# Performance work log

Hardware: AMD Instinct MI355X
Metric: run time of the kernel (lower is better)

The kernel has to match this reference:

```python
import jax, jax.numpy as jnp
import numpy as np

N = 65536        # total points across batch
NS = 16          # nsample (kNN neighbors)
D = 64           # d_model
FF = 64          # dim_feedforward width
CIN = 16         # input feature channels
EPS = 1e-5       # BatchNorm eps


def _bn_relu(x, g, b):
    # BatchNorm1d in training mode: per-channel stats over (N, L); x: (N, C, L)
    m = x.mean(axis=(0, 2), keepdims=True)
    v = x.var(axis=(0, 2), keepdims=True)
    return jax.nn.relu((x - m) * jax.lax.rsqrt(v + EPS) * g[None, :, None] + b[None, :, None])


def _dknn_layer(xyz, feats, knn_idx, knn_empty,
                wq, bq, wk, bk, w1, g1, b1, w2, g2, b2, wo, go, bo):
    # nhead = 1 -> single head uses the full d_model split
    Q = feats @ wq + bq                        # (N, D)
    K = feats @ wk + bk                        # (N, D)
    Kx = jnp.concatenate([K, xyz], axis=1)     # use_xyz=True -> (N, D+3)
    Qx = jnp.concatenate([Q, xyz], axis=1)     # (N, D+3)
    Kg = jnp.transpose(Kx[knn_idx], (0, 2, 1))  # irregular gather -> (N, D+3, NS)
    Qe = Qx[:, :, None]                        # (N, D+3, 1)
    x = jnp.concatenate([Kg - Qe, jnp.broadcast_to(Qe, Kg.shape)], axis=1)  # (N, 2*(D+3), NS)
    x = jnp.where(knn_empty[:, None, None], 0.0, x)   # empty-ball masking
    x = _bn_relu(jnp.einsum('ncs,cf->nfs', x, w1), g1, b1)  # Conv1d k=1 == channel matmul
    x = _bn_relu(jnp.einsum('ncs,cf->nfs', x, w2), g2, b2)
    x = jnp.max(x, axis=2, keepdims=True)      # max-pool over neighbors -> (N, FF, 1)
    x = _bn_relu(jnp.einsum('ncs,cf->nfs', x, wo), go, bo)  # out_conv
    return x[:, :, 0]                          # (N, D)


def setup_inputs() -> dict:
    key = jax.random.key(0)
    ks = jax.random.split(key, 16)
    inp = {
        'src_xyz': jax.random.normal(ks[0], (N, 3), jnp.float32) * 20.0,
        'src_feats': jax.random.normal(ks[1], (N, CIN), jnp.float32),
        'knn_idx': jax.random.randint(ks[2], (N, NS), 0, N, jnp.int32),
        'knn_empty': jax.random.randint(ks[3], (N,), 0, 20, jnp.int32) == 0,
    }
    k = 4
    cin = CIN
    for i in range(2):
        s = 1.0 / np.sqrt(cin)
        inp[f'l{i}_wq'] = jax.random.normal(ks[k], (cin, D), jnp.float32) * s; k += 1
        inp[f'l{i}_bq'] = jnp.zeros((D,), jnp.float32)
        inp[f'l{i}_wk'] = jax.random.normal(ks[k], (cin, D), jnp.float32) * s; k += 1
        inp[f'l{i}_bk'] = jnp.zeros((D,), jnp.float32)
        c = 2 * (D + 3)
        inp[f'l{i}_w1'] = jax.random.normal(ks[k], (c, FF), jnp.float32) * np.sqrt(2.0 / c); k += 1
        inp[f'l{i}_g1'] = jnp.ones((FF,), jnp.float32)
        inp[f'l{i}_b1'] = jnp.zeros((FF,), jnp.float32)
        inp[f'l{i}_w2'] = jax.random.normal(ks[k], (FF, FF), jnp.float32) * np.sqrt(2.0 / FF); k += 1
        inp[f'l{i}_g2'] = jnp.ones((FF,), jnp.float32)
        inp[f'l{i}_b2'] = jnp.zeros((FF,), jnp.float32)
        inp[f'l{i}_wo'] = jax.random.normal(ks[k], (FF, D), jnp.float32) * np.sqrt(2.0 / FF); k += 1
        inp[f'l{i}_go'] = jnp.ones((D,), jnp.float32)
        inp[f'l{i}_bo'] = jnp.zeros((D,), jnp.float32)
        cin = D
    return inp


def reference(src_xyz, src_feats, knn_idx, knn_empty,
              l0_wq, l0_bq, l0_wk, l0_bk, l0_w1, l0_g1, l0_b1, l0_w2, l0_g2, l0_b2, l0_wo, l0_go, l0_bo,
              l1_wq, l1_bq, l1_wk, l1_bk, l1_w1, l1_g1, l1_b1, l1_w2, l1_g2, l1_b2, l1_wo, l1_go, l1_bo):
    f = _dknn_layer(src_xyz, src_feats, knn_idx, knn_empty,
                    l0_wq, l0_bq, l0_wk, l0_bk, l0_w1, l0_g1, l0_b1, l0_w2, l0_g2, l0_b2, l0_wo, l0_go, l0_bo)
    f = _dknn_layer(src_xyz, f, knn_idx, knn_empty,
                    l1_wq, l1_bq, l1_wk, l1_bk, l1_w1, l1_g1, l1_b1, l1_w2, l1_g2, l1_b2, l1_wo, l1_go, l1_bo)
    return f
```

## Files before the change

### kernel.cpp

```cpp
#include <hip/hip_runtime.h>
#include <cstdint>

#define NPTS 65536
#define NS 16
#define EPSV 1e-5f

typedef __attribute__((ext_vector_type(8))) short bf16x8;
typedef __attribute__((ext_vector_type(4))) float f32x4;
typedef __attribute__((ext_vector_type(4))) unsigned int u32x4;
union FragU { u32x4 u; bf16x8 h; };

#define SUM1 0
#define SSQ1 64
#define SUM2 128
#define SSQ2 192
#define SUM3 256
#define SSQ3 320
#define WKAOF 0
#define WQBAOF 4096
#define BKAOF 8192
#define BQBAOF 8256
#define WFOLD_FLOATS 8320

__device__ __forceinline__ void split2(float e0, float e1, unsigned int& hi, unsigned int& lo) {
    unsigned int u0 = __float_as_uint(e0), u1 = __float_as_uint(e1);
    unsigned int h0 = u0 & 0xFFFF0000u, h1 = u1 & 0xFFFF0000u;
    hi = (h0 >> 16) | h1;
    float l0f = e0 - __uint_as_float(h0);
    float l1f = e1 - __uint_as_float(h1);
    lo = (__float_as_uint(l0f) >> 16) | (__float_as_uint(l1f) & 0xFFFF0000u);
}

__global__ void k_mask(const uint32_t* emp32, uint8_t* mask) {
    int bad = 0;
    for (int w = threadIdx.x; w < 1024; w += 256) bad |= (emp32[w] > 1u) ? 1 : 0;
    __shared__ int sbad[4];
    unsigned long long b = __ballot(bad != 0);
    if ((threadIdx.x & 63) == 0) sbad[threadIdx.x >> 6] = (b != 0ull) ? 1 : 0;
    __syncthreads();
    int flag = sbad[0] | sbad[1] | sbad[2] | sbad[3];
    int i = blockIdx.x * 256 + threadIdx.x;
    uint8_t mv;
    if (flag) mv = (((const uint8_t*)emp32)[i] != 0);
    else      mv = (emp32[i] != 0u);
    mask[i] = mv;
}

__global__ void k0(const float* wq, const float* bq, const float* wk, const float* bk,
                   const float* w1, float* wfold, int cin) {
    int f = threadIdx.x;
    int c = blockIdx.x;
    float a = 0.f, q = 0.f;
    for (int d = 0; d < 64; d++) {
        float A  = w1[d*64 + f];
        float Bm = w1[(67+d)*64 + f] - A;
        a = fmaf(wk[c*64 + d], A,  a);
        q = fmaf(wq[c*64 + d], Bm, q);
    }
    wfold[WKAOF  + c*64 + f] = a;
    wfold[WQBAOF + c*64 + f] = q;
    if (c == 0) {
        float ba = 0.f, bqv = 0.f;
        for (int d = 0; d < 64; d++) {
            float A  = w1[d*64 + f];
            float Bm = w1[(67+d)*64 + f] - A;
            ba  = fmaf(bk[d], A,  ba);
            bqv = fmaf(bq[d], Bm, bqv);
        }
        wfold[BKAOF  + f] = ba;
        wfold[BQBAOF + f] = bqv;
    }
}

template<int CIN, bool PREBN>
__global__ void __launch_bounds__(256) k1m(const float* __restrict__ feats, const float* __restrict__ xyz,
                    const float* __restrict__ w1, const float* __restrict__ wfold,
                    const float* __restrict__ statsPrev, const float* __restrict__ goP,
                    const float* __restrict__ boP,
                    float* __restrict__ KA, float* __restrict__ QBA) {
    const int l = threadIdx.x & 63;
    const int wv = threadIdx.x >> 6;
    const int sidx = l & 15;
    const int g = l >> 4;
    const int col = sidx;
    constexpr int NT = (CIN == 64) ? 2 : 1;

    unsigned int bh[NT][2][4], bl[NT][2][4];
    #pragma unroll
    for (int t = 0; t < NT; t++)
    #pragma unroll
    for (int fl = 0; fl < 2; fl++) {
        int f128 = (wv*2 + fl)*16 + col;
        const float* W = (f128 < 64) ? (wfold + WKAOF) : (wfold + WQBAOF);
        int f = (f128 < 64) ? f128 : f128 - 64;
        #pragma unroll
        for (int r = 0; r < 4; r++) {
            int c0 = t*32 + g*8 + 2*r;
            float e0 = 0.f, e1 = 0.f;
            if (CIN == 64 || g < 2) {
                e0 = W[c0*64 + f];
                e1 = W[(c0+1)*64 + f];
            }
            split2(e0, e1, bh[t][fl][r], bl[t][fl][r]);
        }
    }
    unsigned int xbh[2][4], xbl[2][4];
    float biasf[2];
    #pragma unroll
    for (int fl = 0; fl < 2; fl++) {
        int f128 = (wv*2 + fl)*16 + col;
        float A0, A1, A2;
        if (f128 < 64) {
            A0 = w1[64*64 + f128]; A1 = w1[65*64 + f128]; A2 = w1[66*64 + f128];
            biasf[fl] = wfold[BKAOF + f128];
        } else {
            int f = f128 - 64;
            A0 = w1[131*64 + f] - w1[64*64 + f];
            A1 = w1[132*64 + f] - w1[65*64 + f];
            A2 = w1[133*64 + f] - w1[66*64 + f];
            biasf[fl] = wfold[BQBAOF + f];
        }
        split2(A0, A1, xbh[fl][0], xbl[fl][0]);
        split2(A2, 0.f, xbh[fl][1], xbl[fl][1]);
        xbh[fl][2] = 0; xbh[fl][3] = 0; xbl[fl][2] = 0; xbl[fl][3] = 0;
    }
    float scP[NT*8], shP[NT*8];
    if (PREBN) {
        const float invN = 1.0f / (float)NPTS;
        #pragma unroll
        for (int t = 0; t < NT; t++)
        #pragma unroll
        for (int i = 0; i < 8; i++) {
            int c = t*32 + g*8 + i;
            float m = statsPrev[SUM3 + c] * invN;
            float v = fmaxf(statsPrev[SSQ3 + c] * invN - m*m, 0.0f);
            float s = goP[c] * rsqrtf(v + EPSV);
            scP[t*8+i] = s;
            shP[t*8+i] = fmaf(-m, s, boP[c]);
        }
    }

    for (int tile = blockIdx.x; tile < NPTS/16; tile += gridDim.x) {
        int p = tile*16 + sidx;
        unsigned int ahu[NT][4], alu[NT][4];
        #pragma unroll
        for (int t = 0; t < NT; t++) {
            float xv[8];
            if (CIN == 64) {
                f32x4 a0 = *(const f32x4*)(feats + (size_t)p*64 + t*32 + g*8);
                f32x4 a1 = *(const f32x4*)(feats + (size_t)p*64 + t*32 + g*8 + 4);
                #pragma unroll
                for (int i = 0; i < 4; i++) { xv[i] = a0[i]; xv[4+i] = a1[i]; }
                if (PREBN) {
                    #pragma unroll
                    for (int i = 0; i < 8; i++)
                        xv[i] = fmaxf(fmaf(scP[t*8+i], xv[i], shP[t*8+i]), 0.0f);
                }
            } else {
                if (g < 2) {
                    f32x4 a0 = *(const f32x4*)(feats + (size_t)p*16 + g*8);
                    f32x4 a1 = *(const f32x4*)(feats + (size_t)p*16 + g*8 + 4);
                    #pragma unroll
                    for (int i = 0; i < 4; i++) { xv[i] = a0[i]; xv[4+i] = a1[i]; }
                } else {
                    #pragma unroll
                    for (int i = 0; i < 8; i++) xv[i] = 0.f;
                }
            }
            #pragma unroll
            for (int r = 0; r < 4; r++) split2(xv[2*r], xv[2*r+1], ahu[t][r], alu[t][r]);
        }
        unsigned int xah[4] = {0,0,0,0}, xal[4] = {0,0,0,0};
        if (g == 0) {
            float x0 = xyz[p*3], x1 = xyz[p*3+1], x2 = xyz[p*3+2];
            split2(x0, x1, xah[0], xal[0]);
            split2(x2, 0.f, xah[1], xal[1]);
        }
        f32x4 acc[2];
        #pragma unroll
        for (int fl = 0; fl < 2; fl++)
            acc[fl] = (f32x4){biasf[fl], biasf[fl], biasf[fl], biasf[fl]};
        #pragma unroll
        for (int t = 0; t < NT; t++) {
            FragU ah, al;
            ah.u = (u32x4){ahu[t][0], ahu[t][1], ahu[t][2], ahu[t][3]};
            al.u = (u32x4){alu[t][0], alu[t][1], alu[t][2], alu[t][3]};
            #pragma unroll
            for (int fl = 0; fl < 2; fl++) {
                FragU Bh, Bl;
                Bh.u = (u32x4){bh[t][fl][0], bh[t][fl][1], bh[t][fl][2], bh[t][fl][3]};
                Bl.u = (u32x4){bl[t][fl][0], bl[t][fl][1], bl[t][fl][2], bl[t][fl][3]};
                acc[fl] = __builtin_amdgcn_mfma_f32_16x16x32_bf16(ah.h, Bh.h, acc[fl], 0, 0, 0);
                acc[fl] = __builtin_amdgcn_mfma_f32_16x16x32_bf16(ah.h, Bl.h, acc[fl], 0, 0, 0);
                acc[fl] = __builtin_amdgcn_mfma_f32_16x16x32_bf16(al.h, Bh.h, acc[fl], 0, 0, 0);
            }
        }
        {
            FragU ah, al;
            ah.u = (u32x4){xah[0], xah[1], xah[2], xah[3]};
            al.u = (u32x4){xal[0], xal[1], xal[2], xal[3]};
            #pragma unroll
            for (int fl = 0; fl < 2; fl++) {
                FragU Bh, Bl;
                Bh.u = (u32x4){xbh[fl][0], xbh[fl][1], xbh[fl][2], xbh[fl][3]};
                Bl.u = (u32x4){xbl[fl][0], xbl[fl][1], xbl[fl][2], xbl[fl][3]};
                acc[fl] = __builtin_amdgcn_mfma_f32_16x16x32_bf16(ah.h, Bh.h, acc[fl], 0, 0, 0);
                acc[fl] = __builtin_amdgcn_mfma_f32_16x16x32_bf16(ah.h, Bl.h, acc[fl], 0, 0, 0);
                acc[fl] = __builtin_amdgcn_mfma_f32_16x16x32_bf16(al.h, Bh.h, acc[fl], 0, 0, 0);
            }
        }
        #pragma unroll
        for (int fl = 0; fl < 2; fl++) {
            int f128 = (wv*2 + fl)*16 + col;
            #pragma unroll
            for (int r = 0; r < 4; r++) {
                int po = tile*16 + g*4 + r;
                float v = acc[fl][r];
                if (f128 < 64) KA[(size_t)po*64 + f128] = v;
                else           QBA[(size_t)po*64 + (f128-64)] = v;
            }
        }
    }
}

__global__ void __launch_bounds__(256) k2(const float* __restrict__ KA, const float* __restrict__ QBA,
                   const int* __restrict__ knn, const uint8_t* __restrict__ mask, float* stats) {
    const int l = threadIdx.x & 63;
    const int wv = threadIdx.x >> 6;
    const int s = l & 15;
    const int g = l >> 4;
    float s0[16], s1[16];
    #pragma unroll
    for (int i = 0; i < 16; i++) { s0[i] = 0.f; s1[i] = 0.f; }
    for (int n = blockIdx.x * 4 + wv; n < NPTS; n += gridDim.x * 4) {
        if (mask[n]) continue;
        int j = knn[n*16 + s];
        const float* kap = KA + (size_t)j*64 + g*16;
        const float* qbp = QBA + (size_t)n*64 + g*16;
        #pragma unroll
        for (int q = 0; q < 4; q++) {
            f32x4 ka = *(const f32x4*)(kap + q*4);
            f32x4 qb = *(const f32x4*)(qbp + q*4);
            #pragma unroll
            for (int e = 0; e < 4; e++) {
                float y = ka[e] + qb[e];
                s0[q*4+e] += y;
                s1[q*4+e] = fmaf(y, y, s1[q*4+e]);
            }
        }
    }
    #pragma unroll
    for (int i = 0; i < 16; i++) {
        #pragma unroll
        for (int d = 1; d < 16; d <<= 1) {
            s0[i] += __shfl_xor(s0[i], d, 64);
            s1[i] += __shfl_xor(s1[i], d, 64);
        }
    }
    __shared__ float r0[4][64], r1[4][64];
    if (s == 0) {
        #pragma unroll
        for (int i = 0; i < 16; i++) { r0[wv][g*16+i] = s0[i]; r1[wv][g*16+i] = s1[i]; }
    }
    __syncthreads();
    int tid = threadIdx.x;
    if (tid < 64) {
        atomicAdd(&stats[SUM1 + tid], r0[0][tid]+r0[1][tid]+r0[2][tid]+r0[3][tid]);
        atomicAdd(&stats[SSQ1 + tid], r1[0][tid]+r1[1][tid]+r1[2][tid]+r1[3][tid]);
    }
}

__global__ void __launch_bounds__(256) k4(const float* KA, const float* QBA, const int* knn,
                   const uint8_t* mask, const float* w2, const float* g1, const float* b1,
                   float* stats, float* y2max, float* y2min) {
    const int l    = threadIdx.x & 63;
    const int wv   = threadIdx.x >> 6;
    const int sidx = l & 15;
    const int g    = l >> 4;
    const int col  = sidx;

    float sc1v[16], sh1v[16];
    const float inv = 1.0f / ((float)NPTS * (float)NS);
    #pragma unroll
    for (int t = 0; t < 2; t++)
    #pragma unroll
    for (int i = 0; i < 8; i++) {
        int c = t*32 + g*8 + i;
        float m = stats[SUM1 + c] * inv;
        float v = fmaxf(stats[SSQ1 + c] * inv - m*m, 0.0f);
        float s = g1[c] * rsqrtf(v + EPSV);
        sc1v[t*8+i] = s;
        sh1v[t*8+i] = fmaf(-m, s, b1[c]);
    }

    unsigned int whu[2][4][4], wlu[2][4][4];
    #pragma unroll
    for (int t = 0; t < 2; t++)
    #pragma unroll
    for (int ft = 0; ft < 4; ft++)
    #pragma unroll
    for (int r = 0; r < 4; r++) {
        int k0i = t*32 + g*8 + 2*r;
        float e0 = w2[k0i*64 + ft*16 + col];
        float e1 = w2[(k0i+1)*64 + ft*16 + col];
        split2(e0, e1, whu[t][ft][r], wlu[t][ft][r]);
    }

    float s0t[4] = {0.f,0.f,0.f,0.f};
    float s1t[4] = {0.f,0.f,0.f,0.f};

    for (int n = blockIdx.x * 4 + wv; n < NPTS; n += gridDim.x * 4) {
        bool masked = mask[n] != 0;
        int j = knn[n*16 + sidx];

        f32x4 kaA = *(const f32x4*)(KA + (size_t)j*64 + g*8);
        f32x4 kaB = *(const f32x4*)(KA + (size_t)j*64 + g*8 + 4);
        f32x4 kaC = *(const f32x4*)(KA + (size_t)j*64 + 32 + g*8);
        f32x4 kaD = *(const f32x4*)(KA + (size_t)j*64 + 32 + g*8 + 4);
        f32x4 qA  = *(const f32x4*)(QBA + (size_t)n*64 + g*8);
        f32x4 qB  = *(const f32x4*)(QBA + (size_t)n*64 + g*8 + 4);
        f32x4 qC  = *(const f32x4*)(QBA + (size_t)n*64 + 32 + g*8);
        f32x4 qD  = *(const f32x4*)(QBA + (size_t)n*64 + 32 + g*8 + 4);

        float x[16];
        #pragma unroll
        for (int i = 0; i < 4; i++) {
            float y0 = masked ? 0.f : (kaA[i] + qA[i]);
            float y1 = masked ? 0.f : (kaB[i] + qB[i]);
            float y2 = masked ? 0.f : (kaC[i] + qC[i]);
            float y3 = masked ? 0.f : (kaD[i] + qD[i]);
            x[i]    = fmaxf(fmaf(sc1v[i],    y0, sh1v[i]),    0.0f);
            x[4+i]  = fmaxf(fmaf(sc1v[4+i],  y1, sh1v[4+i]),  0.0f);
            x[8+i]  = fmaxf(fmaf(sc1v[8+i],  y2, sh1v[8+i]),  0.0f);
            x[12+i] = fmaxf(fmaf(sc1v[12+i], y3, sh1v[12+i]), 0.0f);
        }

        unsigned int ahu[2][4], alu[2][4];
        #pragma unroll
        for (int t = 0; t < 2; t++)
        #pragma unroll
        for (int r = 0; r < 4; r++)
            split2(x[t*8 + 2*r], x[t*8 + 2*r + 1], ahu[t][r], alu[t][r]);

        f32x4 acc[4];
        #pragma unroll
        for (int ft = 0; ft < 4; ft++) acc[ft] = (f32x4){0.f,0.f,0.f,0.f};

        #pragma unroll
        for (int t = 0; t < 2; t++) {
            FragU ah, al;
            ah.u = (u32x4){ahu[t][0], ahu[t][1], ahu[t][2], ahu[t][3]};
            al.u = (u32x4){alu[t][0], alu[t][1], alu[t][2], alu[t][3]};
            #pragma unroll
            for (int ft = 0; ft < 4; ft++) {
                FragU bhf, blf;
                bhf.u = (u32x4){whu[t][ft][0], whu[t][ft][1], whu[t][ft][2], whu[t][ft][3]};
                blf.u = (u32x4){wlu[t][ft][0], wlu[t][ft][1], wlu[t][ft][2], wlu[t][ft][3]};
                acc[ft] = __builtin_amdgcn_mfma_f32_16x16x32_bf16(ah.h, bhf.h, acc[ft], 0, 0, 0);
                acc[ft] = __builtin_amdgcn_mfma_f32_16x16x32_bf16(ah.h, blf.h, acc[ft], 0, 0, 0);
                acc[ft] = __builtin_amdgcn_mfma_f32_16x16x32_bf16(al.h, bhf.h, acc[ft], 0, 0, 0);
            }
        }

        float tmax[4], tmin[4];
        #pragma unroll
        for (int ft = 0; ft < 4; ft++) {
            f32x4 d = acc[ft];
            float lmax = fmaxf(fmaxf(d[0], d[1]), fmaxf(d[2], d[3]));
            float lmin = fminf(fminf(d[0], d[1]), fminf(d[2], d[3]));
            s0t[ft] += (d[0] + d[1]) + (d[2] + d[3]);
            s1t[ft] += fmaf(d[0],d[0], fmaf(d[1],d[1], fmaf(d[2],d[2], d[3]*d[3])));
            lmax = fmaxf(lmax, __shfl_xor(lmax, 16, 64));
            lmax = fmaxf(lmax, __shfl_xor(lmax, 32, 64));
            lmin = fminf(lmin, __shfl_xor(lmin, 16, 64));
            lmin = fminf(lmin, __shfl_xor(lmin, 32, 64));
            tmax[ft] = lmax; tmin[ft] = lmin;
        }
        float mx = (g==0) ? tmax[0] : (g==1) ? tmax[1] : (g==2) ? tmax[2] : tmax[3];
        float mn = (g==0) ? tmin[0] : (g==1) ? tmin[1] : (g==2) ? tmin[2] : tmin[3];
        y2max[(size_t)n*64 + l] = mx;
        y2min[(size_t)n*64 + l] = mn;
    }

    #pragma unroll
    for (int ft = 0; ft < 4; ft++) {
        s0t[ft] += __shfl_xor(s0t[ft], 16, 64);
        s0t[ft] += __shfl_xor(s0t[ft], 32, 64);
        s1t[ft] += __shfl_xor(s1t[ft], 16, 64);
        s1t[ft] += __shfl_xor(s1t[ft], 32, 64);
    }
    float myS0 = (g==0) ? s0t[0] : (g==1) ? s0t[1] : (g==2) ? s0t[2] : s0t[3];
    float myS1 = (g==0) ? s1t[0] : (g==1) ? s1t[1] : (g==2) ? s1t[2] : s1t[3];
    __shared__ float red[8][64];
    red[wv][l] = myS0;
    red[4+wv][l] = myS1;
    __syncthreads();
    if (wv == 0) {
        atomicAdd(&stats[SUM2 + l], red[0][l]+red[1][l]+red[2][l]+red[3][l]);
        atomicAdd(&stats[SSQ2 + l], red[4][l]+red[5][l]+red[6][l]+red[7][l]);
    }
}

__global__ void __launch_bounds__(256) k5m(const float* __restrict__ y2max, const float* __restrict__ y2min,
                    const float* __restrict__ wo, const float* __restrict__ g2, const float* __restrict__ b2,
                    float* stats, float* __restrict__ y3) {
    const int l = threadIdx.x & 63;
    const int wv = threadIdx.x >> 6;
    const int sidx = l & 15;
    const int g = l >> 4;
    const int ft = wv;

    unsigned int bh[2][4], bl[2][4];
    #pragma unroll
    for (int t = 0; t < 2; t++)
    #pragma unroll
    for (int r = 0; r < 4; r++) {
        int c0 = t*32 + g*8 + 2*r;
        split2(wo[c0*64 + ft*16 + sidx], wo[(c0+1)*64 + ft*16 + sidx], bh[t][r], bl[t][r]);
    }
    float sc2v[16], sh2v[16];
    const float inv = 1.0f / ((float)NPTS * (float)NS);
    #pragma unroll
    for (int t = 0; t < 2; t++)
    #pragma unroll
    for (int i = 0; i < 8; i++) {
        int c = t*32 + g*8 + i;
        float m = stats[SUM2 + c] * inv;
        float v = fmaxf(stats[SSQ2 + c] * inv - m*m, 0.0f);
        float s = g2[c] * rsqrtf(v + EPSV);
        sc2v[t*8+i] = s;
        sh2v[t*8+i] = fmaf(-m, s, b2[c]);
    }
    float s0a = 0.f, s1a = 0.f;
    for (int tile = blockIdx.x; tile < NPTS/16; tile += gridDim.x) {
        int p = tile*16 + sidx;
        unsigned int ahu[2][4], alu[2][4];
        #pragma unroll
        for (int t = 0; t < 2; t++) {
            f32x4 mx0 = *(const f32x4*)(y2max + (size_t)p*64 + t*32 + g*8);
            f32x4 mx1 = *(const f32x4*)(y2max + (size_t)p*64 + t*32 + g*8 + 4);
            f32x4 mn0 = *(const f32x4*)(y2min + (size_t)p*64 + t*32 + g*8);
            f32x4 mn1 = *(const f32x4*)(y2min + (size_t)p*64 + t*32 + g*8 + 4);
            float mval[8];
            #pragma unroll
            for (int i = 0; i < 4; i++) {
                float sc = sc2v[t*8+i];
                float pre = (sc >= 0.f) ? mx0[i] : mn0[i];
                mval[i] = fmaxf(fmaf(sc, pre, sh2v[t*8+i]), 0.0f);
                float sc2 = sc2v[t*8+4+i];
                float pre2 = (sc2 >= 0.f) ? mx1[i] : mn1[i];
                mval[4+i] = fmaxf(fmaf(sc2, pre2, sh2v[t*8+4+i]), 0.0f);
            }
            #pragma unroll
            for (int r = 0; r < 4; r++) split2(mval[2*r], mval[2*r+1], ahu[t][r], alu[t][r]);
        }
        f32x4 acc = (f32x4){0.f,0.f,0.f,0.f};
        #pragma unroll
        for (int t = 0; t < 2; t++) {
            FragU ah, al, Bh, Bl;
            ah.u = (u32x4){ahu[t][0], ahu[t][1], ahu[t][2], ahu[t][3]};
            al.u = (u32x4){alu[t][0], alu[t][1], alu[t][2], alu[t][3]};
            Bh.u = (u32x4){bh[t][0], bh[t][1], bh[t][2], bh[t][3]};
            Bl.u = (u32x4){bl[t][0], bl[t][1], bl[t][2], bl[t][3]};
            acc = __builtin_amdgcn_mfma_f32_16x16x32_bf16(ah.h, Bh.h, acc, 0, 0, 0);
            acc = __builtin_amdgcn_mfma_f32_16x16x32_bf16(ah.h, Bl.h, acc, 0, 0, 0);
            acc = __builtin_amdgcn_mfma_f32_16x16x32_bf16(al.h, Bh.h, acc, 0, 0, 0);
        }
        #pragma unroll
        for (int r = 0; r < 4; r++) {
            int po = tile*16 + g*4 + r;
            float v = acc[r];
            y3[(size_t)po*64 + ft*16 + sidx] = v;
            s0a += v;
            s1a = fmaf(v, v, s1a);
        }
    }
    s0a += __shfl_xor(s0a, 16, 64); s0a += __shfl_xor(s0a, 32, 64);
    s1a += __shfl_xor(s1a, 16, 64); s1a += __shfl_xor(s1a, 32, 64);
    __shared__ float r0[64], r1[64];
    if (l < 16) { r0[wv*16 + sidx] = s0a; r1[wv*16 + sidx] = s1a; }
    __syncthreads();
    int tid = threadIdx.x;
    if (tid < 64) {
        atomicAdd(&stats[SUM3 + tid], r0[tid]);
        atomicAdd(&stats[SSQ3 + tid], r1[tid]);
    }
}

__global__ void k6(float* y3, const float* stats, const float* go, const float* bo) {
    int i = blockIdx.x * 256 + threadIdx.x;
    int f = i & 63;
    const float inv = 1.0f / (float)NPTS;
    float m = stats[SUM3 + f] * inv;
    float v = fmaxf(stats[SSQ3 + f] * inv - m*m, 0.0f);
    float s = go[f] * rsqrtf(v + EPSV);
    float sh = fmaf(-m, s, bo[f]);
    y3[i] = fmaxf(fmaf(s, y3[i], sh), 0.0f);
}

extern "C" void kernel_launch(void* const* d_in, const int* in_sizes, int n_in,
                              void* d_out, int out_size, void* d_ws, size_t ws_size,
                              hipStream_t stream) {
    const float* xyz    = (const float*)d_in[0];
    const float* feats0 = (const float*)d_in[1];
    const int*   knn    = (const int*)d_in[2];
    const void*  empty  = d_in[3];
    float* ws = (float*)d_ws;
    const size_t N64 = (size_t)NPTS * 64;
    float* KA    = ws;
    float* QBA   = ws + N64;
    float* Y2MAX = ws + 2*N64;
    float* Y2MIN = ws + 3*N64;
    float* stats = ws + 4*N64;
    float* wfold = stats + 1024;
    uint8_t* mask = (uint8_t*)(wfold + WFOLD_FLOATS);
    float* out = (float*)d_out;

    hipMemsetAsync(stats, 0, 1024 * sizeof(float), stream);
    k_mask<<<NPTS/256, 256, 0, stream>>>((const uint32_t*)empty, mask);

    const float* const* p0 = (const float* const*)(d_in + 4);
    const float* const* p1 = (const float* const*)(d_in + 4 + 13);

    {
        const float* const* p = p0;
        float* sl = stats;
        k0<<<16, 64, 0, stream>>>(p[0], p[1], p[2], p[3], p[4], wfold, 16);
        k1m<16, false><<<1024, 256, 0, stream>>>(feats0, xyz, p[4], wfold,
                                                 sl, p[11], p[12], KA, QBA);
        k2<<<2048, 256, 0, stream>>>(KA, QBA, knn, mask, sl);
        k4<<<2048, 256, 0, stream>>>(KA, QBA, knn, mask, p[7], p[5], p[6], sl, Y2MAX, Y2MIN);
        k5m<<<2048, 256, 0, stream>>>(Y2MAX, Y2MIN, p[10], p[8], p[9], sl, out);
    }
    {
        const float* const* p = p1;
        float* sl = stats + 512;
        k0<<<64, 64, 0, stream>>>(p[0], p[1], p[2], p[3], p[4], wfold, 64);
        k1m<64, true><<<1024, 256, 0, stream>>>(out, xyz, p[4], wfold,
                                                stats, p0[11], p0[12], KA, QBA);
        k2<<<2048, 256, 0, stream>>>(KA, QBA, knn, mask, sl);
        k4<<<2048, 256, 0, stream>>>(KA, QBA, knn, mask, p[7], p[5], p[6], sl, Y2MAX, Y2MIN);
        k5m<<<2048, 256, 0, stream>>>(Y2MAX, Y2MIN, p[10], p[8], p[9], sl, out);
        k6<<<NPTS*64/256, 256, 0, stream>>>(out, sl, p[11], p[12]);
    }
}
```

Before: 621.3 us.

## Prefetch next point's neighbor gather and precompute masked-point result in k2/k4

k2 and k4 now software-pipeline the irregular KA gather, loading the next point's neighbor rows while the current point is processed. k4 precomputes the constant output for masked (empty-ball) points once per thread and reuses it instead of running the MFMA chain for them. The split2 helper packs bf16 halves with a byte-permute instruction, the kernels gain occupancy hints and restrict qualifiers, and their grids are halved so each wave loops over more points. The prefetch adds register pressure, which the occupancy hint may turn into spills.

Measured after the change: 752.4 us. +21.1%, slower.

```diff
diff --git a/kernel.cpp b/kernel.cpp
--- a/kernel.cpp
+++ b/kernel.cpp
@@ -24,11 +24,10 @@
 
 __device__ __forceinline__ void split2(float e0, float e1, unsigned int& hi, unsigned int& lo) {
     unsigned int u0 = __float_as_uint(e0), u1 = __float_as_uint(e1);
-    unsigned int h0 = u0 & 0xFFFF0000u, h1 = u1 & 0xFFFF0000u;
-    hi = (h0 >> 16) | h1;
-    float l0f = e0 - __uint_as_float(h0);
-    float l1f = e1 - __uint_as_float(h1);
-    lo = (__float_as_uint(l0f) >> 16) | (__float_as_uint(l1f) & 0xFFFF0000u);
+    hi = __builtin_amdgcn_perm(u1, u0, 0x07060302u);
+    float l0f = e0 - __uint_as_float(u0 & 0xFFFF0000u);
+    float l1f = e1 - __uint_as_float(u1 & 0xFFFF0000u);
+    lo = __builtin_amdgcn_perm(__float_as_uint(l1f), __float_as_uint(l0f), 0x07060302u);
 }
 
 __global__ void k_mask(const uint32_t* emp32, uint8_t* mask) {
@@ -223,7 +222,7 @@
     }
 }
 
-__global__ void __launch_bounds__(256) k2(const float* __restrict__ KA, const float* __restrict__ QBA,
+__global__ void __launch_bounds__(256, 4) k2(const float* __restrict__ KA, const float* __restrict__ QBA,
                    const int* __restrict__ knn, const uint8_t* __restrict__ mask, float* stats) {
     const int l = threadIdx.x & 63;
     const int wv = threadIdx.x >> 6;
@@ -232,22 +231,56 @@
     float s0[16], s1[16];
     #pragma unroll
     for (int i = 0; i < 16; i++) { s0[i] = 0.f; s1[i] = 0.f; }
-    for (int n = blockIdx.x * 4 + wv; n < NPTS; n += gridDim.x * 4) {
-        if (mask[n]) continue;
-        int j = knn[n*16 + s];
-        const float* kap = KA + (size_t)j*64 + g*16;
-        const float* qbp = QBA + (size_t)n*64 + g*16;
-        #pragma unroll
-        for (int q = 0; q < 4; q++) {
-            f32x4 ka = *(const f32x4*)(kap + q*4);
-            f32x4 qb = *(const f32x4*)(qbp + q*4);
+
+    const int STR = gridDim.x * 4;
+    int n0 = blockIdx.x * 4 + wv;
+    bool mC = true;
+    f32x4 ka0{}, ka1{}, ka2{}, ka3{};
+    if (n0 < NPTS) {
+        mC = (mask[n0] != 0);
+        if (!mC) {
+            int j = knn[n0*16 + s];
+            const float* kap = KA + (size_t)j*64 + g*16;
+            ka0 = *(const f32x4*)(kap);
+            ka1 = *(const f32x4*)(kap + 4);
+            ka2 = *(const f32x4*)(kap + 8);
+            ka3 = *(const f32x4*)(kap + 12);
+        }
+    }
+    for (int n = n0; n < NPTS; n += STR) {
+        int nn = n + STR;
+        bool mN = true;
+        f32x4 nk0{}, nk1{}, nk2{}, nk3{};
+        if (nn < NPTS) {
+            mN = (mask[nn] != 0);
+            if (!mN) {
+                int j = knn[nn*16 + s];
+                const float* kap = KA + (size_t)j*64 + g*16;
+                nk0 = *(const f32x4*)(kap);
+                nk1 = *(const f32x4*)(kap + 4);
+                nk2 = *(const f32x4*)(kap + 8);
+                nk3 = *(const f32x4*)(kap + 12);
+            }
+        }
+        if (!mC) {
+            const float* qbp = QBA + (size_t)n*64 + g*16;
+            f32x4 qb0 = *(const f32x4*)(qbp);
+            f32x4 qb1 = *(const f32x4*)(qbp + 4);
+            f32x4 qb2 = *(const f32x4*)(qbp + 8);
+            f32x4 qb3 = *(const f32x4*)(qbp + 12);
             #pragma unroll
             for (int e = 0; e < 4; e++) {
-                float y = ka[e] + qb[e];
-                s0[q*4+e] += y;
-                s1[q*4+e] = fmaf(y, y, s1[q*4+e]);
-            }
-        }
+                float y0 = ka0[e] + qb0[e];
+                float y1 = ka1[e] + qb1[e];
+                float y2 = ka2[e] + qb2[e];
+                float y3 = ka3[e] + qb3[e];
+                s0[e]    += y0;  s1[e]    = fmaf(y0, y0, s1[e]);
+                s0[4+e]  += y1;  s1[4+e]  = fmaf(y1, y1, s1[4+e]);
+                s0[8+e]  += y2;  s1[8+e]  = fmaf(y2, y2, s1[8+e]);
+                s0[12+e] += y3;  s1[12+e] = fmaf(y3, y3, s1[12+e]);
+            }
+        }
+        mC = mN; ka0 = nk0; ka1 = nk1; ka2 = nk2; ka3 = nk3;
     }
     #pragma unroll
     for (int i = 0; i < 16; i++) {
@@ -270,9 +303,10 @@
     }
 }
 
-__global__ void __launch_bounds__(256) k4(const float* KA, const float* QBA, const int* knn,
-                   const uint8_t* mask, const float* w2, const float* g1, const float* b1,
-                   float* stats, float* y2max, float* y2min) {
+__global__ void __launch_bounds__(256, 4) k4(const float* __restrict__ KA, const float* __restrict__ QBA,
+                   const int* __restrict__ knn, const uint8_t* __restrict__ mask,
+                   const float* __restrict__ w2, const float* __restrict__ g1, const float* __restrict__ b1,
+                   float* stats, float* __restrict__ y2max, float* __restrict__ y2min) {
     const int l    = threadIdx.x & 63;
     const int wv   = threadIdx.x >> 6;
     const int sidx = l & 15;
@@ -306,80 +340,148 @@
         split2(e0, e1, whu[t][ft][r], wlu[t][ft][r]);
     }
 
-    float s0t[4] = {0.f,0.f,0.f,0.f};
-    float s1t[4] = {0.f,0.f,0.f,0.f};
-
-    for (int n = blockIdx.x * 4 + wv; n < NPTS; n += gridDim.x * 4) {
-        bool masked = mask[n] != 0;
-        int j = knn[n*16 + sidx];
-
-        f32x4 kaA = *(const f32x4*)(KA + (size_t)j*64 + g*8);
-        f32x4 kaB = *(const f32x4*)(KA + (size_t)j*64 + g*8 + 4);
-        f32x4 kaC = *(const f32x4*)(KA + (size_t)j*64 + 32 + g*8);
-        f32x4 kaD = *(const f32x4*)(KA + (size_t)j*64 + 32 + g*8 + 4);
-        f32x4 qA  = *(const f32x4*)(QBA + (size_t)n*64 + g*8);
-        f32x4 qB  = *(const f32x4*)(QBA + (size_t)n*64 + g*8 + 4);
-        f32x4 qC  = *(const f32x4*)(QBA + (size_t)n*64 + 32 + g*8);
-        f32x4 qD  = *(const f32x4*)(QBA + (size_t)n*64 + 32 + g*8 + 4);
-
-        float x[16];
-        #pragma unroll
-        for (int i = 0; i < 4; i++) {
-            float y0 = masked ? 0.f : (kaA[i] + qA[i]);
-            float y1 = masked ? 0.f : (kaB[i] + qB[i]);
-            float y2 = masked ? 0.f : (kaC[i] + qC[i]);
-            float y3 = masked ? 0.f : (kaD[i] + qD[i]);
-            x[i]    = fmaxf(fmaf(sc1v[i],    y0, sh1v[i]),    0.0f);
-            x[4+i]  = fmaxf(fmaf(sc1v[4+i],  y1, sh1v[4+i]),  0.0f);
-            x[8+i]  = fmaxf(fmaf(sc1v[8+i],  y2, sh1v[8+i]),  0.0f);
-            x[12+i] = fmaxf(fmaf(sc1v[12+i], y3, sh1v[12+i]), 0.0f);
-        }
-
-        unsigned int ahu[2][4], alu[2][4];
+    float s0M[4], s1M[4], mxM, mnM;
+    {
+        f32x4 accM[4];
+        #pragma unroll
+        for (int ft = 0; ft < 4; ft++) accM[ft] = (f32x4){0.f,0.f,0.f,0.f};
+        unsigned int mhu[2][4], mlu[2][4];
         #pragma unroll
         for (int t = 0; t < 2; t++)
         #pragma unroll
         for (int r = 0; r < 4; r++)
-            split2(x[t*8 + 2*r], x[t*8 + 2*r + 1], ahu[t][r], alu[t][r]);
-
-        f32x4 acc[4];
-        #pragma unroll
-        for (int ft = 0; ft < 4; ft++) acc[ft] = (f32x4){0.f,0.f,0.f,0.f};
-
+            split2(fmaxf(sh1v[t*8+2*r], 0.0f), fmaxf(sh1v[t*8+2*r+1], 0.0f), mhu[t][r], mlu[t][r]);
         #pragma unroll
         for (int t = 0; t < 2; t++) {
             FragU ah, al;
-            ah.u = (u32x4){ahu[t][0], ahu[t][1], ahu[t][2], ahu[t][3]};
-            al.u = (u32x4){alu[t][0], alu[t][1], alu[t][2], alu[t][3]};
+            ah.u = (u32x4){mhu[t][0], mhu[t][1], mhu[t][2], mhu[t][3]};
+            al.u = (u32x4){mlu[t][0], mlu[t][1], mlu[t][2], mlu[t][3]};
             #pragma unroll
             for (int ft = 0; ft < 4; ft++) {
                 FragU bhf, blf;
                 bhf.u = (u32x4){whu[t][ft][0], whu[t][ft][1], whu[t][ft][2], whu[t][ft][3]};
                 blf.u = (u32x4){wlu[t][ft][0], wlu[t][ft][1], wlu[t][ft][2], wlu[t][ft][3]};
-                acc[ft] = __builtin_amdgcn_mfma_f32_16x16x32_bf16(ah.h, bhf.h, acc[ft], 0, 0, 0);
-                acc[ft] = __builtin_amdgcn_mfma_f32_16x16x32_bf16(ah.h, blf.h, acc[ft], 0, 0, 0);
-                acc[ft] = __builtin_amdgcn_mfma_f32_16x16x32_bf16(al.h, bhf.h, acc[ft], 0, 0, 0);
-            }
-        }
-
-        float tmax[4], tmin[4];
+                accM[ft] = __builtin_amdgcn_mfma_f32_16x16x32_bf16(ah.h, bhf.h, accM[ft], 0, 0, 0);
+                accM[ft] = __builtin_amdgcn_mfma_f32_16x16x32_bf16(ah.h, blf.h, accM[ft], 0, 0, 0);
+                accM[ft] = __builtin_amdgcn_mfma_f32_16x16x32_bf16(al.h, bhf.h, accM[ft], 0, 0, 0);
+            }
+        }
+        float tmaxM[4], tminM[4];
         #pragma unroll
         for (int ft = 0; ft < 4; ft++) {
-            f32x4 d = acc[ft];
+            f32x4 d = accM[ft];
+            s0M[ft] = (d[0] + d[1]) + (d[2] + d[3]);
+            s1M[ft] = fmaf(d[0],d[0], fmaf(d[1],d[1], fmaf(d[2],d[2], d[3]*d[3])));
             float lmax = fmaxf(fmaxf(d[0], d[1]), fmaxf(d[2], d[3]));
             float lmin = fminf(fminf(d[0], d[1]), fminf(d[2], d[3]));
-            s0t[ft] += (d[0] + d[1]) + (d[2] + d[3]);
-            s1t[ft] += fmaf(d[0],d[0], fmaf(d[1],d[1], fmaf(d[2],d[2], d[3]*d[3])));
             lmax = fmaxf(lmax, __shfl_xor(lmax, 16, 64));
             lmax = fmaxf(lmax, __shfl_xor(lmax, 32, 64));
             lmin = fminf(lmin, __shfl_xor(lmin, 16, 64));
             lmin = fminf(lmin, __shfl_xor(lmin, 32, 64));
-            tmax[ft] = lmax; tmin[ft] = lmin;
-        }
-        float mx = (g==0) ? tmax[0] : (g==1) ? tmax[1] : (g==2) ? tmax[2] : tmax[3];
-        float mn = (g==0) ? tmin[0] : (g==1) ? tmin[1] : (g==2) ? tmin[2] : tmin[3];
-        y2max[(size_t)n*64 + l] = mx;
-        y2min[(size_t)n*64 + l] = mn;
+            tmaxM[ft] = lmax; tminM[ft] = lmin;
+        }
+        mxM = (g==0) ? tmaxM[0] : (g==1) ? tmaxM[1] : (g==2) ? tmaxM[2] : tmaxM[3];
+        mnM = (g==0) ? tminM[0] : (g==1) ? tminM[1] : (g==2) ? tminM[2] : tminM[3];
+    }
+
+    float s0t[4] = {0.f,0.f,0.f,0.f};
+    float s1t[4] = {0.f,0.f,0.f,0.f};
+
+    const int STR = gridDim.x * 4;
+    int n0 = blockIdx.x * 4 + wv;
+    bool mC = true;
+    f32x4 ka0{}, ka1{}, ka2{}, ka3{};
+    if (n0 < NPTS) {
+        mC = (mask[n0] != 0);
+        if (!mC) {
+            int j = knn[n0*16 + sidx];
+            ka0 = *(const f32x4*)(KA + (size_t)j*64 + g*8);
+            ka1 = *(const f32x4*)(KA + (size_t)j*64 + g*8 + 4);
+            ka2 = *(const f32x4*)(KA + (size_t)j*64 + 32 + g*8);
+            ka3 = *(const f32x4*)(KA + (size_t)j*64 + 32 + g*8 + 4);
+        }
+    }
+    for (int n = n0; n < NPTS; n += STR) {
+        int nn = n + STR;
+        bool mN = true;
+        f32x4 nk0{}, nk1{}, nk2{}, nk3{};
+        if (nn < NPTS) {
+            mN = (mask[nn] != 0);
+            if (!mN) {
+                int j = knn[nn*16 + sidx];
+                nk0 = *(const f32x4*)(KA + (size_t)j*64 + g*8);
+                nk1 = *(const f32x4*)(KA + (size_t)j*64 + g*8 + 4);
+                nk2 = *(const f32x4*)(KA + (size_t)j*64 + 32 + g*8);
+                nk3 = *(const f32x4*)(KA + (size_t)j*64 + 32 + g*8 + 4);
+            }
+        }
+        if (mC) {
+            #pragma unroll
+            for (int ft = 0; ft < 4; ft++) { s0t[ft] += s0M[ft]; s1t[ft] += s1M[ft]; }
+            y2max[(size_t)n*64 + l] = mxM;
+            y2min[(size_t)n*64 + l] = mnM;
+        } else {
+            f32x4 qA = *(const f32x4*)(QBA + (size_t)n*64 + g*8);
+            f32x4 qB = *(const f32x4*)(QBA + (size_t)n*64 + g*8 + 4);
+            f32x4 qC = *(const f32x4*)(QBA + (size_t)n*64 + 32 + g*8);
+            f32x4 qD = *(const f32x4*)(QBA + (size_t)n*64 + 32 + g*8 + 4);
+
+            float x[16];
+            #pragma unroll
+            for (int i = 0; i < 4; i++) {
+                x[i]    = fmaxf(fmaf(sc1v[i],    ka0[i] + qA[i], sh1v[i]),    0.0f);
+                x[4+i]  = fmaxf(fmaf(sc1v[4+i],  ka1[i] + qB[i], sh1v[4+i]),  0.0f);
+                x[8+i]  = fmaxf(fmaf(sc1v[8+i],  ka2[i] + qC[i], sh1v[8+i]),  0.0f);
+                x[12+i] = fmaxf(fmaf(sc1v[12+i], ka3[i] + qD[i], sh1v[12+i]), 0.0f);
+            }
+
+            unsigned int ahu[2][4], alu[2][4];
+            #pragma unroll
+            for (int t = 0; t < 2; t++)
+            #pragma unroll
+            for (int r = 0; r < 4; r++)
+                split2(x[t*8 + 2*r], x[t*8 + 2*r + 1], ahu[t][r], alu[t][r]);
+
+            f32x4 acc[4];
+            #pragma unroll
+            for (int ft = 0; ft < 4; ft++) acc[ft] = (f32x4){0.f,0.f,0.f,0.f};
+
+            #pragma unroll
+            for (int t = 0; t < 2; t++) {
+                FragU ah, al;
+                ah.u = (u32x4){ahu[t][0], ahu[t][1], ahu[t][2], ahu[t][3]};
+                al.u = (u32x4){alu[t][0], alu[t][1], alu[t][2], alu[t][3]};
+                #pragma unroll
+                for (int ft = 0; ft < 4; ft++) {
+                    FragU bhf, blf;
+                    bhf.u = (u32x4){whu[t][ft][0], whu[t][ft][1], whu[t][ft][2], whu[t][ft][3]};
+                    blf.u = (u32x4){wlu[t][ft][0], wlu[t][ft][1], wlu[t][ft][2], wlu[t][ft][3]};
+                    acc[ft] = __builtin_amdgcn_mfma_f32_16x16x32_bf16(ah.h, bhf.h, acc[ft], 0, 0, 0);
+                    acc[ft] = __builtin_amdgcn_mfma_f32_16x16x32_bf16(ah.h, blf.h, acc[ft], 0, 0, 0);
+                    acc[ft] = __builtin_amdgcn_mfma_f32_16x16x32_bf16(al.h, bhf.h, acc[ft], 0, 0, 0);
+                }
+            }
+
+            float tmax[4], tmin[4];
+            #pragma unroll
+            for (int ft = 0; ft < 4; ft++) {
+                f32x4 d = acc[ft];
+                float lmax = fmaxf(fmaxf(d[0], d[1]), fmaxf(d[2], d[3]));
+                float lmin = fminf(fminf(d[0], d[1]), fminf(d[2], d[3]));
+                s0t[ft] += (d[0] + d[1]) + (d[2] + d[3]);
+                s1t[ft] += fmaf(d[0],d[0], fmaf(d[1],d[1], fmaf(d[2],d[2], d[3]*d[3])));
+                lmax = fmaxf(lmax, __shfl_xor(lmax, 16, 64));
+                lmax = fmaxf(lmax, __shfl_xor(lmax, 32, 64));
+                lmin = fminf(lmin, __shfl_xor(lmin, 16, 64));
+                lmin = fminf(lmin, __shfl_xor(lmin, 32, 64));
+                tmax[ft] = lmax; tmin[ft] = lmin;
+            }
+            float mx = (g==0) ? tmax[0] : (g==1) ? tmax[1] : (g==2) ? tmax[2] : tmax[3];
+            float mn = (g==0) ? tmin[0] : (g==1) ? tmin[1] : (g==2) ? tmin[2] : tmin[3];
+            y2max[(size_t)n*64 + l] = mx;
+            y2min[(size_t)n*64 + l] = mn;
+        }
+        mC = mN; ka0 = nk0; ka1 = nk1; ka2 = nk2; ka3 = nk3;
     }
 
     #pragma unroll
@@ -528,8 +630,8 @@
         k0<<<16, 64, 0, stream>>>(p[0], p[1], p[2], p[3], p[4], wfold, 16);
         k1m<16, false><<<1024, 256, 0, stream>>>(feats0, xyz, p[4], wfold,
                                                  sl, p[11], p[12], KA, QBA);
-        k2<<<2048, 256, 0, stream>>>(KA, QBA, knn, mask, sl);
-        k4<<<2048, 256, 0, stream>>>(KA, QBA, knn, mask, p[7], p[5], p[6], sl, Y2MAX, Y2MIN);
+        k2<<<1024, 256, 0, stream>>>(KA, QBA, knn, mask, sl);
+        k4<<<1024, 256, 0, stream>>>(KA, QBA, knn, mask, p[7], p[5], p[6], sl, Y2MAX, Y2MIN);
         k5m<<<2048, 256, 0, stream>>>(Y2MAX, Y2MIN, p[10], p[8], p[9], sl, out);
     }
     {
@@ -538,8 +640,8 @@
         k0<<<64, 64, 0, stream>>>(p[0], p[1], p[2], p[3], p[4], wfold, 64);
         k1m<64, true><<<1024, 256, 0, stream>>>(out, xyz, p[4], wfold,
                                                 stats, p0[11], p0[12], KA, QBA);
-        k2<<<2048, 256, 0, stream>>>(KA, QBA, knn, mask, sl);
-        k4<<<2048, 256, 0, stream>>>(KA, QBA, knn, mask, p[7], p[5], p[6], sl, Y2MAX, Y2MIN);
+        k2<<<1024, 256, 0, stream>>>(KA, QBA, knn, mask, sl);
+        k4<<<1024, 256, 0, stream>>>(KA, QBA, knn, mask, p[7], p[5], p[6], sl, Y2MAX, Y2MIN);
         k5m<<<2048, 256, 0, stream>>>(Y2MAX, Y2MIN, p[10], p[8], p[9], sl, out);
         k6<<<NPTS*64/256, 256, 0, stream>>>(out, sl, p[11], p[12]);
     }
```
